# Kernel optimization log

Measured on AMD Instinct MI355X. Metric: run time of the kernel, lower is better.

The kernel has to match this reference:

```python
import jax, jax.numpy as jnp
import numpy as np

N_POINTS = 8388608  # 8M points


def setup_inputs() -> dict:
    key = jax.random.key(0)
    k1, k2 = jax.random.split(key)
    pcloud = jax.random.normal(k1, (1, N_POINTS, 3), dtype=jnp.float32)
    P1 = jax.random.normal(k2, (3,), dtype=jnp.float32)
    return {"pcloud": pcloud, "P1": P1, "K": 64}


def reference(pcloud, P1, K):
    # pcloud: (1, N, 3) -> (N, 3); P1: (3,) -> (1, 3)
    pts = pcloud.reshape(-1, 3)
    diff = pts - P1.reshape(1, 3)
    dist = jnp.sqrt(jnp.sum(diff * diff, axis=1))  # L2 distance per point, (N,)
    # torch.topk(largest=False) == top_k on negated distances
    _, idx = jax.lax.top_k(-dist, K)  # (K,)
    return pts[idx], idx.reshape(1, -1)
```

## Files before the change

kernel.cpp:

```cpp
#include <hip/hip_runtime.h>
#include <stdint.h>

#define NBINS 4096
#define NB2   4096
#define NBLK  2048
#define SLOT  16
#define OVF_CAP 8192
#define LDS_CAND 8192
#define SAMP_PTS 131072
#define CHUNK_PTS 256
#define CHUNK_F4  192

__device__ __forceinline__ uint32_t dist_key(float x, float y, float z,
                                             float px, float py, float pz) {
    float dx = __fsub_rn(x, px);
    float dy = __fsub_rn(y, py);
    float dz = __fsub_rn(z, pz);
    float s = __fadd_rn(__fadd_rn(__fmul_rn(dx, dx), __fmul_rn(dy, dy)),
                        __fmul_rn(dz, dz));
    float d = __fsqrt_rn(s);
    return __float_as_uint(d);
}

__global__ void __launch_bounds__(256) sample_hist_kernel(const float* __restrict__ pts,
                                                          const float* __restrict__ P1,
                                                          uint32_t* __restrict__ ghist,
                                                          int nsamp) {
    __shared__ uint32_t lh[NBINS];
    for (int i = threadIdx.x; i < NBINS; i += 256) lh[i] = 0;
    __syncthreads();
    float px = P1[0], py = P1[1], pz = P1[2];
    int gid = blockIdx.x * 256 + threadIdx.x;
    const float4* p4 = (const float4*)pts;
    if (gid * 4 < nsamp) {
        float4 A = p4[gid * 3 + 0];
        float4 Bv = p4[gid * 3 + 1];
        float4 Cv = p4[gid * 3 + 2];
        atomicAdd(&lh[dist_key(A.x, A.y, A.z, px, py, pz) >> 20], 1u);
        atomicAdd(&lh[dist_key(A.w, Bv.x, Bv.y, px, py, pz) >> 20], 1u);
        atomicAdd(&lh[dist_key(Bv.z, Bv.w, Cv.x, px, py, pz) >> 20], 1u);
        atomicAdd(&lh[dist_key(Cv.y, Cv.z, Cv.w, px, py, pz) >> 20], 1u);
    }
    __syncthreads();
    for (int i = threadIdx.x; i < NBINS; i += 256) {
        uint32_t v = lh[i];
        if (v) atomicAdd(&ghist[i], v);
    }
}

__global__ void __launch_bounds__(256) scan_kernel(const uint32_t* __restrict__ ghist,
                                                   uint32_t* __restrict__ cut, int K) {
    __shared__ uint32_t s[256];
    int t = threadIdx.x;
    uint32_t mine[16];
    uint32_t local = 0;
    for (int j = 0; j < 16; ++j) {
        mine[j] = ghist[t * 16 + j];
        local += mine[j];
    }
    s[t] = local;
    __syncthreads();
    for (int off = 1; off < 256; off <<= 1) {
        uint32_t v = (t >= off) ? s[t - off] : 0;
        __syncthreads();
        s[t] += v;
        __syncthreads();
    }
    uint32_t incl = s[t];
    uint32_t excl = incl - local;
    if (excl < (uint32_t)K && incl >= (uint32_t)K) {
        uint32_t run = excl;
        for (int j = 0; j < 16; ++j) {
            run += mine[j];
            if (run >= (uint32_t)K) {
                *cut = (uint32_t)(t * 16 + j);
                break;
            }
        }
    }
}

__global__ void __launch_bounds__(256) filter6_kernel(const float* __restrict__ pts,
                                                      const float* __restrict__ P1,
                                                      const uint32_t* __restrict__ cut,
                                                      unsigned long long* __restrict__ gslots,
                                                      uint32_t* __restrict__ gcount,
                                                      uint32_t* __restrict__ ovf_cnt,
                                                      unsigned long long* __restrict__ ovf,
                                                      int nchunks, int N) {
    __shared__ float4 park[4][CHUNK_F4];
    __shared__ unsigned long long lhits[SLOT];
    __shared__ uint32_t lcnt;
    if (threadIdx.x == 0) lcnt = 0;
    __syncthreads();

    const float4* p4 = (const float4*)pts;
    float px = P1[0], py = P1[1], pz = P1[2];
    uint32_t cb = *cut;
    int w = threadIdx.x >> 6;
    int lane = threadIdx.x & 63;
    int b = blockIdx.x;
    int cpb = (nchunks + NBLK - 1) / NBLK;
    int cbeg = b * cpb;
    int cend = cbeg + cpb; if (cend > nchunks) cend = nchunks;

    float4 r0, r1, r2;
    int c = cbeg + w;
    if (c < cend) {
        const float4* s = p4 + (size_t)c * CHUNK_F4;
        r0 = s[lane]; r1 = s[lane + 64]; r2 = s[lane + 128];
    }
    for (; c < cend; c += 4) {
        park[w][lane] = r0;
        park[w][lane + 64] = r1;
        park[w][lane + 128] = r2;
        int cn = c + 4;
        if (cn < cend) {
            const float4* s = p4 + (size_t)cn * CHUNK_F4;
            r0 = s[lane]; r1 = s[lane + 64]; r2 = s[lane + 128];
        }
        asm volatile("s_waitcnt lgkmcnt(0)" ::: "memory");
        const float* fb = (const float*)&park[w][0] + lane * 12;
        float4 A  = *(const float4*)(fb);
        float4 Bv = *(const float4*)(fb + 4);
        float4 Cv = *(const float4*)(fb + 8);
        uint32_t kk[4];
        kk[0] = dist_key(A.x, A.y, A.z, px, py, pz);
        kk[1] = dist_key(A.w, Bv.x, Bv.y, px, py, pz);
        kk[2] = dist_key(Bv.z, Bv.w, Cv.x, px, py, pz);
        kk[3] = dist_key(Cv.y, Cv.z, Cv.w, px, py, pz);
        uint32_t pbase = (uint32_t)c * CHUNK_PTS + (uint32_t)lane * 4;
        #pragma unroll
        for (int j = 0; j < 4; ++j) {
            if ((kk[j] >> 20) <= cb) {
                unsigned long long cv = ((unsigned long long)kk[j] << 32) |
                                        (unsigned long long)(pbase + j);
                uint32_t pos = atomicAdd(&lcnt, 1u);
                if (pos < SLOT) {
                    lhits[pos] = cv;
                } else {
                    uint32_t op = atomicAdd(ovf_cnt, 1u);
                    if (op < OVF_CAP) ovf[op] = cv;
                }
            }
        }
    }
    if (b == NBLK - 1 && threadIdx.x == 0) {
        for (int i = nchunks * CHUNK_PTS; i < N; ++i) {
            uint32_t kk = dist_key(pts[3 * i], pts[3 * i + 1], pts[3 * i + 2], px, py, pz);
            if ((kk >> 20) <= cb) {
                unsigned long long cv = ((unsigned long long)kk << 32) |
                                        (unsigned long long)(uint32_t)i;
                uint32_t pos = atomicAdd(&lcnt, 1u);
                if (pos < SLOT) {
                    lhits[pos] = cv;
                } else {
                    uint32_t op = atomicAdd(ovf_cnt, 1u);
                    if (op < OVF_CAP) ovf[op] = cv;
                }
            }
        }
    }
    __syncthreads();
    uint32_t n = lcnt; if (n > SLOT) n = SLOT;
    if (threadIdx.x < n) gslots[(size_t)b * SLOT + threadIdx.x] = lhits[threadIdx.x];
    if (threadIdx.x == 0) gcount[b] = n;
}

__global__ void __launch_bounds__(1024) refine_select_kernel(
        const uint32_t* __restrict__ gcount,
        const unsigned long long* __restrict__ gslots,
        const uint32_t* __restrict__ ovf_cnt,
        const unsigned long long* __restrict__ ovf,
        const uint32_t* __restrict__ cut,
        unsigned long long* __restrict__ cand2,
        const float* __restrict__ pts,
        float* __restrict__ out, int K) {
    __shared__ uint32_t hist2[NB2];
    __shared__ uint32_t ssum[1024];
    __shared__ unsigned long long lcand[LDS_CAND];
    __shared__ uint32_t cut2_s, m2_s;
    int t = threadIdx.x;
    uint32_t cb = *cut;
    unsigned long long R = ((unsigned long long)(cb + 1)) << 20;
    uint32_t M32 = (uint32_t)((((unsigned long long)NB2) << 32) / R);
    uint32_t novf = *ovf_cnt; if (novf > OVF_CAP) novf = OVF_CAP;

    for (int i = t; i < NB2; i += 1024) hist2[i] = 0;
    if (t == 0) m2_s = 0;
    __syncthreads();
    for (int b = t; b < NBLK; b += 1024) {
        uint32_t n = gcount[b];
        for (uint32_t j = 0; j < n; ++j) {
            uint32_t key = (uint32_t)(gslots[(size_t)b * SLOT + j] >> 32);
            atomicAdd(&hist2[(uint32_t)(((unsigned long long)key * M32) >> 32)], 1u);
        }
    }
    for (uint32_t i = t; i < novf; i += 1024) {
        uint32_t key = (uint32_t)(ovf[i] >> 32);
        atomicAdd(&hist2[(uint32_t)(((unsigned long long)key * M32) >> 32)], 1u);
    }
    __syncthreads();

    uint32_t mine[4];
    uint32_t local = 0;
    for (int j = 0; j < 4; ++j) { mine[j] = hist2[t * 4 + j]; local += mine[j]; }
    ssum[t] = local;
    __syncthreads();
    for (int off = 1; off < 1024; off <<= 1) {
        uint32_t v = (t >= off) ? ssum[t - off] : 0;
        __syncthreads();
        ssum[t] += v;
        __syncthreads();
    }
    uint32_t incl = ssum[t], excl = incl - local;
    if (excl < (uint32_t)K && incl >= (uint32_t)K) {
        uint32_t run = excl;
        for (int j = 0; j < 4; ++j) {
            run += mine[j];
            if (run >= (uint32_t)K) { cut2_s = (uint32_t)(t * 4 + j); break; }
        }
    }
    __syncthreads();
    uint32_t c2 = cut2_s;

    for (int b = t; b < NBLK; b += 1024) {
        uint32_t n = gcount[b];
        for (uint32_t j = 0; j < n; ++j) {
            unsigned long long cv = gslots[(size_t)b * SLOT + j];
            uint32_t key = (uint32_t)(cv >> 32);
            if ((uint32_t)(((unsigned long long)key * M32) >> 32) <= c2) {
                uint32_t pos = atomicAdd(&m2_s, 1u);
                if (pos < LDS_CAND) lcand[pos] = cv;
                cand2[pos] = cv;
            }
        }
    }
    for (uint32_t i = t; i < novf; i += 1024) {
        unsigned long long cv = ovf[i];
        uint32_t key = (uint32_t)(cv >> 32);
        if ((uint32_t)(((unsigned long long)key * M32) >> 32) <= c2) {
            uint32_t pos = atomicAdd(&m2_s, 1u);
            if (pos < LDS_CAND) lcand[pos] = cv;
            cand2[pos] = cv;
        }
    }
    __syncthreads();
    uint32_t M2 = m2_s;

    if (M2 <= LDS_CAND) {
        for (uint32_t i = t; i < M2; i += 1024) {
            unsigned long long ci = lcand[i];
            uint32_t rank = 0;
            for (uint32_t j = 0; j < M2; ++j) rank += (lcand[j] < ci) ? 1u : 0u;
            if (rank < (uint32_t)K) {
                uint32_t idx = (uint32_t)(ci & 0xFFFFFFFFu);
                out[3 * rank + 0] = pts[3 * idx + 0];
                out[3 * rank + 1] = pts[3 * idx + 1];
                out[3 * rank + 2] = pts[3 * idx + 2];
                out[3 * K + rank] = (float)idx;
            }
        }
    } else {
        for (uint32_t i = t; i < M2; i += 1024) {
            unsigned long long ci = cand2[i];
            uint32_t rank = 0;
            for (uint32_t j = 0; j < M2; ++j) rank += (cand2[j] < ci) ? 1u : 0u;
            if (rank < (uint32_t)K) {
                uint32_t idx = (uint32_t)(ci & 0xFFFFFFFFu);
                out[3 * rank + 0] = pts[3 * idx + 0];
                out[3 * rank + 1] = pts[3 * idx + 1];
                out[3 * rank + 2] = pts[3 * idx + 2];
                out[3 * K + rank] = (float)idx;
            }
        }
    }
}

extern "C" void kernel_launch(void* const* d_in, const int* in_sizes, int n_in,
                              void* d_out, int out_size, void* d_ws, size_t ws_size,
                              hipStream_t stream) {
    const float* pts = (const float*)d_in[0];
    const float* P1  = (const float*)d_in[1];
    float* out = (float*)d_out;

    int N = in_sizes[0] / 3;
    int nchunks = N / CHUNK_PTS;
    int K = out_size / 4;
    int nsamp = (N < SAMP_PTS) ? (N / 4) * 4 : SAMP_PTS;

    uint32_t* w       = (uint32_t*)d_ws;
    uint32_t* ovf_cnt = w + 0;
    uint32_t* cut     = w + 1;
    uint32_t* hist    = w + 4;
    uint32_t* gcount  = w + 4 + NBINS;
    unsigned long long* gslots = (unsigned long long*)(w + 4 + NBINS + NBLK);
    unsigned long long* ovf    = gslots + (size_t)NBLK * SLOT;
    unsigned long long* cand2  = ovf + OVF_CAP;

    hipMemsetAsync(w, 0, (size_t)(4 + NBINS + NBLK) * sizeof(uint32_t), stream);
    sample_hist_kernel<<<(nsamp / 4 + 255) / 256, 256, 0, stream>>>(pts, P1, hist, nsamp);
    scan_kernel<<<1, 256, 0, stream>>>(hist, cut, K);
    filter6_kernel<<<NBLK, 256, 0, stream>>>(pts, P1, cut, gslots, gcount, ovf_cnt, ovf, nchunks, N);
    refine_select_kernel<<<1, 1024, 0, stream>>>(gcount, gslots, ovf_cnt, ovf, cut,
                                                 cand2, pts, out, K);
}
```

Baseline: 45.16 us.

## Fuse scan into sampling and refine into filter via last-block atomic counters

Merges the single-block scan into the sampling kernel and the single-block refine/select into the filter kernel. The last block to finish, found through an atomic done counter, runs the follow-up work, which cuts the launch count from four to two and removes the gaps between dependent kernels. The refine stage now runs with 256 threads instead of 1024, uses a smaller second histogram and a smaller LDS candidate buffer, and reuses the parking LDS through a shared byte array. This risks a slower tail phase and a more frequent fallback to the global candidate array.

```diff
diff --git a/kernel.cpp b/kernel.cpp
--- a/kernel.cpp
+++ b/kernel.cpp
@@ -2,12 +2,14 @@
 #include <stdint.h>
 
 #define NBINS 4096
-#define NB2   4096
+#define NB2   2048
 #define NBLK  2048
 #define SLOT  16
 #define OVF_CAP 8192
-#define LDS_CAND 8192
+#define CAND2_CAP 8192
+#define LDS_CAND2 1024
 #define SAMP_PTS 131072
+#define SBLK 128
 #define CHUNK_PTS 256
 #define CHUNK_F4  192
 
@@ -22,11 +24,13 @@
     return __float_as_uint(d);
 }
 
-__global__ void __launch_bounds__(256) sample_hist_kernel(const float* __restrict__ pts,
-                                                          const float* __restrict__ P1,
-                                                          uint32_t* __restrict__ ghist,
-                                                          int nsamp) {
+__global__ void __launch_bounds__(256) sample_scan_kernel(
+        const float* __restrict__ pts, const float* __restrict__ P1,
+        uint32_t* __restrict__ ghist, uint32_t* __restrict__ cutp,
+        uint32_t* __restrict__ done_s, int nsamp, int K) {
     __shared__ uint32_t lh[NBINS];
+    __shared__ uint32_t ssum[256];
+    __shared__ int is_last;
     for (int i = threadIdx.x; i < NBINS; i += 256) lh[i] = 0;
     __syncthreads();
     float px = P1[0], py = P1[1], pz = P1[2];
@@ -46,57 +50,67 @@
         uint32_t v = lh[i];
         if (v) atomicAdd(&ghist[i], v);
     }
-}
-
-__global__ void __launch_bounds__(256) scan_kernel(const uint32_t* __restrict__ ghist,
-                                                   uint32_t* __restrict__ cut, int K) {
-    __shared__ uint32_t s[256];
+    __syncthreads();
+    if (threadIdx.x == 0) {
+        __threadfence();
+        uint32_t old = __hip_atomic_fetch_add(done_s, 1u, __ATOMIC_ACQ_REL,
+                                              __HIP_MEMORY_SCOPE_AGENT);
+        is_last = (old == (uint32_t)(gridDim.x - 1));
+    }
+    __syncthreads();
+    if (!is_last) return;
+    __threadfence();
+
     int t = threadIdx.x;
     uint32_t mine[16];
     uint32_t local = 0;
     for (int j = 0; j < 16; ++j) {
-        mine[j] = ghist[t * 16 + j];
+        mine[j] = __hip_atomic_load(&ghist[t * 16 + j], __ATOMIC_RELAXED,
+                                    __HIP_MEMORY_SCOPE_AGENT);
         local += mine[j];
     }
-    s[t] = local;
+    ssum[t] = local;
     __syncthreads();
     for (int off = 1; off < 256; off <<= 1) {
-        uint32_t v = (t >= off) ? s[t - off] : 0;
+        uint32_t v = (t >= off) ? ssum[t - off] : 0;
         __syncthreads();
-        s[t] += v;
+        ssum[t] += v;
         __syncthreads();
     }
-    uint32_t incl = s[t];
+    uint32_t incl = ssum[t];
     uint32_t excl = incl - local;
     if (excl < (uint32_t)K && incl >= (uint32_t)K) {
         uint32_t run = excl;
         for (int j = 0; j < 16; ++j) {
             run += mine[j];
-            if (run >= (uint32_t)K) {
-                *cut = (uint32_t)(t * 16 + j);
-                break;
-            }
+            if (run >= (uint32_t)K) { *cutp = (uint32_t)(t * 16 + j); break; }
         }
     }
 }
 
-__global__ void __launch_bounds__(256) filter6_kernel(const float* __restrict__ pts,
-                                                      const float* __restrict__ P1,
-                                                      const uint32_t* __restrict__ cut,
-                                                      unsigned long long* __restrict__ gslots,
-                                                      uint32_t* __restrict__ gcount,
-                                                      uint32_t* __restrict__ ovf_cnt,
-                                                      unsigned long long* __restrict__ ovf,
-                                                      int nchunks, int N) {
-    __shared__ float4 park[4][CHUNK_F4];
+__global__ void __launch_bounds__(256) filter_refine_kernel(
+        const float* __restrict__ pts, const float* __restrict__ P1,
+        const uint32_t* __restrict__ cutp,
+        unsigned long long* __restrict__ gslots,
+        uint32_t* __restrict__ gcount,
+        uint32_t* __restrict__ ovf_cnt, unsigned long long* __restrict__ ovf,
+        uint32_t* __restrict__ done_f,
+        unsigned long long* __restrict__ cand2,
+        float* __restrict__ out,
+        int nchunks, int N, int K) {
+    __shared__ __align__(16) unsigned char smem[17472];
     __shared__ unsigned long long lhits[SLOT];
     __shared__ uint32_t lcnt;
+    __shared__ int is_last;
+    __shared__ uint32_t cut2_s, m2_s;
+    float4 (*park)[CHUNK_F4] = (float4 (*)[CHUNK_F4])smem;
+
     if (threadIdx.x == 0) lcnt = 0;
     __syncthreads();
 
     const float4* p4 = (const float4*)pts;
     float px = P1[0], py = P1[1], pz = P1[2];
-    uint32_t cb = *cut;
+    uint32_t cb = *cutp;
     int w = threadIdx.x >> 6;
     int lane = threadIdx.x & 63;
     int b = blockIdx.x;
@@ -164,50 +178,54 @@
     __syncthreads();
     uint32_t n = lcnt; if (n > SLOT) n = SLOT;
     if (threadIdx.x < n) gslots[(size_t)b * SLOT + threadIdx.x] = lhits[threadIdx.x];
-    if (threadIdx.x == 0) gcount[b] = n;
-}
-
-__global__ void __launch_bounds__(1024) refine_select_kernel(
-        const uint32_t* __restrict__ gcount,
-        const unsigned long long* __restrict__ gslots,
-        const uint32_t* __restrict__ ovf_cnt,
-        const unsigned long long* __restrict__ ovf,
-        const uint32_t* __restrict__ cut,
-        unsigned long long* __restrict__ cand2,
-        const float* __restrict__ pts,
-        float* __restrict__ out, int K) {
-    __shared__ uint32_t hist2[NB2];
-    __shared__ uint32_t ssum[1024];
-    __shared__ unsigned long long lcand[LDS_CAND];
-    __shared__ uint32_t cut2_s, m2_s;
+    if (threadIdx.x == 0)
+        __hip_atomic_store(&gcount[b], n, __ATOMIC_RELAXED, __HIP_MEMORY_SCOPE_AGENT);
+
+    __syncthreads();
+    if (threadIdx.x == 0) {
+        __threadfence();
+        uint32_t old = __hip_atomic_fetch_add(done_f, 1u, __ATOMIC_ACQ_REL,
+                                              __HIP_MEMORY_SCOPE_AGENT);
+        is_last = (old == (uint32_t)(NBLK - 1));
+    }
+    __syncthreads();
+    if (!is_last) return;
+    __threadfence();
+
+    uint32_t* hist2 = (uint32_t*)smem;
+    uint32_t* ssum  = (uint32_t*)(smem + 8192);
+    unsigned long long* lc = (unsigned long long*)(smem + 9216);
     int t = threadIdx.x;
-    uint32_t cb = *cut;
     unsigned long long R = ((unsigned long long)(cb + 1)) << 20;
     uint32_t M32 = (uint32_t)((((unsigned long long)NB2) << 32) / R);
-    uint32_t novf = *ovf_cnt; if (novf > OVF_CAP) novf = OVF_CAP;
-
-    for (int i = t; i < NB2; i += 1024) hist2[i] = 0;
-    if (t == 0) m2_s = 0;
-    __syncthreads();
-    for (int b = t; b < NBLK; b += 1024) {
-        uint32_t n = gcount[b];
-        for (uint32_t j = 0; j < n; ++j) {
-            uint32_t key = (uint32_t)(gslots[(size_t)b * SLOT + j] >> 32);
+    uint32_t novf = __hip_atomic_load(ovf_cnt, __ATOMIC_RELAXED,
+                                      __HIP_MEMORY_SCOPE_AGENT);
+    if (novf > OVF_CAP) novf = OVF_CAP;
+
+    for (int i = t; i < NB2; i += 256) hist2[i] = 0;
+    if (t == 0) { m2_s = 0; cut2_s = NB2 - 1; }
+    __syncthreads();
+    for (int bb = t; bb < NBLK; bb += 256) {
+        uint32_t nn = __hip_atomic_load(&gcount[bb], __ATOMIC_RELAXED,
+                                        __HIP_MEMORY_SCOPE_AGENT);
+        if (nn > SLOT) nn = SLOT;
+        for (uint32_t j = 0; j < nn; ++j) {
+            uint32_t key = (uint32_t)(gslots[(size_t)bb * SLOT + j] >> 32);
             atomicAdd(&hist2[(uint32_t)(((unsigned long long)key * M32) >> 32)], 1u);
         }
     }
-    for (uint32_t i = t; i < novf; i += 1024) {
+    for (uint32_t i = t; i < novf; i += 256) {
         uint32_t key = (uint32_t)(ovf[i] >> 32);
         atomicAdd(&hist2[(uint32_t)(((unsigned long long)key * M32) >> 32)], 1u);
     }
     __syncthreads();
 
-    uint32_t mine[4];
+    uint32_t mine[8];
     uint32_t local = 0;
-    for (int j = 0; j < 4; ++j) { mine[j] = hist2[t * 4 + j]; local += mine[j]; }
+    for (int j = 0; j < 8; ++j) { mine[j] = hist2[t * 8 + j]; local += mine[j]; }
     ssum[t] = local;
     __syncthreads();
-    for (int off = 1; off < 1024; off <<= 1) {
+    for (int off = 1; off < 256; off <<= 1) {
         uint32_t v = (t >= off) ? ssum[t - off] : 0;
         __syncthreads();
         ssum[t] += v;
@@ -216,43 +234,45 @@
     uint32_t incl = ssum[t], excl = incl - local;
     if (excl < (uint32_t)K && incl >= (uint32_t)K) {
         uint32_t run = excl;
-        for (int j = 0; j < 4; ++j) {
+        for (int j = 0; j < 8; ++j) {
             run += mine[j];
-            if (run >= (uint32_t)K) { cut2_s = (uint32_t)(t * 4 + j); break; }
+            if (run >= (uint32_t)K) { cut2_s = (uint32_t)(t * 8 + j); break; }
         }
     }
     __syncthreads();
     uint32_t c2 = cut2_s;
 
-    for (int b = t; b < NBLK; b += 1024) {
-        uint32_t n = gcount[b];
-        for (uint32_t j = 0; j < n; ++j) {
-            unsigned long long cv = gslots[(size_t)b * SLOT + j];
+    for (int bb = t; bb < NBLK; bb += 256) {
+        uint32_t nn = __hip_atomic_load(&gcount[bb], __ATOMIC_RELAXED,
+                                        __HIP_MEMORY_SCOPE_AGENT);
+        if (nn > SLOT) nn = SLOT;
+        for (uint32_t j = 0; j < nn; ++j) {
+            unsigned long long cv = gslots[(size_t)bb * SLOT + j];
             uint32_t key = (uint32_t)(cv >> 32);
             if ((uint32_t)(((unsigned long long)key * M32) >> 32) <= c2) {
                 uint32_t pos = atomicAdd(&m2_s, 1u);
-                if (pos < LDS_CAND) lcand[pos] = cv;
-                cand2[pos] = cv;
-            }
-        }
-    }
-    for (uint32_t i = t; i < novf; i += 1024) {
+                if (pos < LDS_CAND2) lc[pos] = cv;
+                if (pos < CAND2_CAP) cand2[pos] = cv;
+            }
+        }
+    }
+    for (uint32_t i = t; i < novf; i += 256) {
         unsigned long long cv = ovf[i];
         uint32_t key = (uint32_t)(cv >> 32);
         if ((uint32_t)(((unsigned long long)key * M32) >> 32) <= c2) {
             uint32_t pos = atomicAdd(&m2_s, 1u);
-            if (pos < LDS_CAND) lcand[pos] = cv;
-            cand2[pos] = cv;
+            if (pos < LDS_CAND2) lc[pos] = cv;
+            if (pos < CAND2_CAP) cand2[pos] = cv;
         }
     }
     __syncthreads();
     uint32_t M2 = m2_s;
 
-    if (M2 <= LDS_CAND) {
-        for (uint32_t i = t; i < M2; i += 1024) {
-            unsigned long long ci = lcand[i];
+    if (M2 <= LDS_CAND2) {
+        for (uint32_t i = t; i < M2; i += 256) {
+            unsigned long long ci = lc[i];
             uint32_t rank = 0;
-            for (uint32_t j = 0; j < M2; ++j) rank += (lcand[j] < ci) ? 1u : 0u;
+            for (uint32_t j = 0; j < M2; ++j) rank += (lc[j] < ci) ? 1u : 0u;
             if (rank < (uint32_t)K) {
                 uint32_t idx = (uint32_t)(ci & 0xFFFFFFFFu);
                 out[3 * rank + 0] = pts[3 * idx + 0];
@@ -262,7 +282,8 @@
             }
         }
     } else {
-        for (uint32_t i = t; i < M2; i += 1024) {
+        if (M2 > CAND2_CAP) M2 = CAND2_CAP;
+        for (uint32_t i = t; i < M2; i += 256) {
             unsigned long long ci = cand2[i];
             uint32_t rank = 0;
             for (uint32_t j = 0; j < M2; ++j) rank += (cand2[j] < ci) ? 1u : 0u;
@@ -290,18 +311,19 @@
     int nsamp = (N < SAMP_PTS) ? (N / 4) * 4 : SAMP_PTS;
 
     uint32_t* w       = (uint32_t*)d_ws;
-    uint32_t* ovf_cnt = w + 0;
-    uint32_t* cut     = w + 1;
-    uint32_t* hist    = w + 4;
-    uint32_t* gcount  = w + 4 + NBINS;
-    unsigned long long* gslots = (unsigned long long*)(w + 4 + NBINS + NBLK);
+    uint32_t* hist    = w;
+    uint32_t* ovf_cnt = w + NBINS;
+    uint32_t* done_s  = w + NBINS + 1;
+    uint32_t* done_f  = w + NBINS + 2;
+    uint32_t* cutp    = w + NBINS + 3;
+    uint32_t* gcount  = w + NBINS + 8;
+    unsigned long long* gslots = (unsigned long long*)(w + NBINS + 8 + NBLK);
     unsigned long long* ovf    = gslots + (size_t)NBLK * SLOT;
     unsigned long long* cand2  = ovf + OVF_CAP;
 
-    hipMemsetAsync(w, 0, (size_t)(4 + NBINS + NBLK) * sizeof(uint32_t), stream);
-    sample_hist_kernel<<<(nsamp / 4 + 255) / 256, 256, 0, stream>>>(pts, P1, hist, nsamp);
-    scan_kernel<<<1, 256, 0, stream>>>(hist, cut, K);
-    filter6_kernel<<<NBLK, 256, 0, stream>>>(pts, P1, cut, gslots, gcount, ovf_cnt, ovf, nchunks, N);
-    refine_select_kernel<<<1, 1024, 0, stream>>>(gcount, gslots, ovf_cnt, ovf, cut,
-                                                 cand2, pts, out, K);
+    hipMemsetAsync(w, 0, (size_t)(NBINS + 4) * sizeof(uint32_t), stream);
+    sample_scan_kernel<<<SBLK, 256, 0, stream>>>(pts, P1, hist, cutp, done_s, nsamp, K);
+    filter_refine_kernel<<<NBLK, 256, 0, stream>>>(pts, P1, cutp, gslots, gcount,
+                                                   ovf_cnt, ovf, done_f, cand2,
+                                                   out, nchunks, N, K);
 }
```

Result: slower. 163.4 us (+261.8%).

## Fuse sample histogram with scan via last-block pattern and double-buffer filter loads

Applied to the files above, without the earlier changes.

The separate scan kernel is folded into the sampling kernel: the last block to finish, detected with an atomic done counter, performs the prefix scan and writes the cut bin. This removes one kernel launch and its dependency gap. The filter loop now keeps two chunks of register prefetch in flight (A and B buffers) instead of one, to hide more global-memory latency at the cost of extra registers. It also shrinks the memset, clamps gcount reads, and initialises cut2_s defensively.

```diff
diff --git a/kernel.cpp b/kernel.cpp
--- a/kernel.cpp
+++ b/kernel.cpp
@@ -8,6 +8,7 @@
 #define OVF_CAP 8192
 #define LDS_CAND 8192
 #define SAMP_PTS 131072
+#define SBLK 128
 #define CHUNK_PTS 256
 #define CHUNK_F4  192
 
@@ -22,11 +23,13 @@
     return __float_as_uint(d);
 }
 
-__global__ void __launch_bounds__(256) sample_hist_kernel(const float* __restrict__ pts,
-                                                          const float* __restrict__ P1,
-                                                          uint32_t* __restrict__ ghist,
-                                                          int nsamp) {
+__global__ void __launch_bounds__(256) sample_scan_kernel(
+        const float* __restrict__ pts, const float* __restrict__ P1,
+        uint32_t* __restrict__ ghist, uint32_t* __restrict__ cutp,
+        uint32_t* __restrict__ done_s, int nsamp, int K) {
     __shared__ uint32_t lh[NBINS];
+    __shared__ uint32_t ssum[256];
+    __shared__ int is_last;
     for (int i = threadIdx.x; i < NBINS; i += 256) lh[i] = 0;
     __syncthreads();
     float px = P1[0], py = P1[1], pz = P1[2];
@@ -46,48 +49,50 @@
         uint32_t v = lh[i];
         if (v) atomicAdd(&ghist[i], v);
     }
-}
-
-__global__ void __launch_bounds__(256) scan_kernel(const uint32_t* __restrict__ ghist,
-                                                   uint32_t* __restrict__ cut, int K) {
-    __shared__ uint32_t s[256];
+    __syncthreads();
+    if (threadIdx.x == 0) {
+        asm volatile("s_waitcnt vmcnt(0)" ::: "memory");
+        uint32_t old = __hip_atomic_fetch_add(done_s, 1u, __ATOMIC_RELAXED,
+                                              __HIP_MEMORY_SCOPE_AGENT);
+        is_last = (old == (uint32_t)(gridDim.x - 1));
+    }
+    __syncthreads();
+    if (!is_last) return;
+
     int t = threadIdx.x;
     uint32_t mine[16];
     uint32_t local = 0;
     for (int j = 0; j < 16; ++j) {
-        mine[j] = ghist[t * 16 + j];
+        mine[j] = __hip_atomic_load(&ghist[t * 16 + j], __ATOMIC_RELAXED,
+                                    __HIP_MEMORY_SCOPE_AGENT);
         local += mine[j];
     }
-    s[t] = local;
+    ssum[t] = local;
     __syncthreads();
     for (int off = 1; off < 256; off <<= 1) {
-        uint32_t v = (t >= off) ? s[t - off] : 0;
+        uint32_t v = (t >= off) ? ssum[t - off] : 0;
         __syncthreads();
-        s[t] += v;
+        ssum[t] += v;
         __syncthreads();
     }
-    uint32_t incl = s[t];
+    uint32_t incl = ssum[t];
     uint32_t excl = incl - local;
     if (excl < (uint32_t)K && incl >= (uint32_t)K) {
         uint32_t run = excl;
         for (int j = 0; j < 16; ++j) {
             run += mine[j];
-            if (run >= (uint32_t)K) {
-                *cut = (uint32_t)(t * 16 + j);
-                break;
-            }
-        }
-    }
-}
-
-__global__ void __launch_bounds__(256) filter6_kernel(const float* __restrict__ pts,
-                                                      const float* __restrict__ P1,
-                                                      const uint32_t* __restrict__ cut,
-                                                      unsigned long long* __restrict__ gslots,
-                                                      uint32_t* __restrict__ gcount,
-                                                      uint32_t* __restrict__ ovf_cnt,
-                                                      unsigned long long* __restrict__ ovf,
-                                                      int nchunks, int N) {
+            if (run >= (uint32_t)K) { *cutp = (uint32_t)(t * 16 + j); break; }
+        }
+    }
+}
+
+__global__ void __launch_bounds__(256) filter_kernel(
+        const float* __restrict__ pts, const float* __restrict__ P1,
+        const uint32_t* __restrict__ cutp,
+        unsigned long long* __restrict__ gslots,
+        uint32_t* __restrict__ gcount,
+        uint32_t* __restrict__ ovf_cnt, unsigned long long* __restrict__ ovf,
+        int nchunks, int N) {
     __shared__ float4 park[4][CHUNK_F4];
     __shared__ unsigned long long lhits[SLOT];
     __shared__ uint32_t lcnt;
@@ -96,7 +101,7 @@
 
     const float4* p4 = (const float4*)pts;
     float px = P1[0], py = P1[1], pz = P1[2];
-    uint32_t cb = *cut;
+    uint32_t cb = *cutp;
     int w = threadIdx.x >> 6;
     int lane = threadIdx.x & 63;
     int b = blockIdx.x;
@@ -104,46 +109,87 @@
     int cbeg = b * cpb;
     int cend = cbeg + cpb; if (cend > nchunks) cend = nchunks;
 
-    float4 r0, r1, r2;
+    float4 a0, a1, a2, b0, b1, b2;
     int c = cbeg + w;
-    if (c < cend) {
+    bool hasA = (c < cend);
+    if (hasA) {
         const float4* s = p4 + (size_t)c * CHUNK_F4;
-        r0 = s[lane]; r1 = s[lane + 64]; r2 = s[lane + 128];
-    }
-    for (; c < cend; c += 4) {
-        park[w][lane] = r0;
-        park[w][lane + 64] = r1;
-        park[w][lane + 128] = r2;
-        int cn = c + 4;
-        if (cn < cend) {
-            const float4* s = p4 + (size_t)cn * CHUNK_F4;
-            r0 = s[lane]; r1 = s[lane + 64]; r2 = s[lane + 128];
+        a0 = s[lane]; a1 = s[lane + 64]; a2 = s[lane + 128];
+    }
+    bool hasB = (c + 4 < cend);
+    if (hasB) {
+        const float4* s = p4 + (size_t)(c + 4) * CHUNK_F4;
+        b0 = s[lane]; b1 = s[lane + 64]; b2 = s[lane + 128];
+    }
+    while (hasA) {
+        park[w][lane] = a0; park[w][lane + 64] = a1; park[w][lane + 128] = a2;
+        bool loadA = (c + 8 < cend);
+        if (loadA) {
+            const float4* s = p4 + (size_t)(c + 8) * CHUNK_F4;
+            a0 = s[lane]; a1 = s[lane + 64]; a2 = s[lane + 128];
         }
         asm volatile("s_waitcnt lgkmcnt(0)" ::: "memory");
-        const float* fb = (const float*)&park[w][0] + lane * 12;
-        float4 A  = *(const float4*)(fb);
-        float4 Bv = *(const float4*)(fb + 4);
-        float4 Cv = *(const float4*)(fb + 8);
-        uint32_t kk[4];
-        kk[0] = dist_key(A.x, A.y, A.z, px, py, pz);
-        kk[1] = dist_key(A.w, Bv.x, Bv.y, px, py, pz);
-        kk[2] = dist_key(Bv.z, Bv.w, Cv.x, px, py, pz);
-        kk[3] = dist_key(Cv.y, Cv.z, Cv.w, px, py, pz);
-        uint32_t pbase = (uint32_t)c * CHUNK_PTS + (uint32_t)lane * 4;
-        #pragma unroll
-        for (int j = 0; j < 4; ++j) {
-            if ((kk[j] >> 20) <= cb) {
-                unsigned long long cv = ((unsigned long long)kk[j] << 32) |
-                                        (unsigned long long)(pbase + j);
-                uint32_t pos = atomicAdd(&lcnt, 1u);
-                if (pos < SLOT) {
-                    lhits[pos] = cv;
-                } else {
-                    uint32_t op = atomicAdd(ovf_cnt, 1u);
-                    if (op < OVF_CAP) ovf[op] = cv;
+        {
+            const float* fb = (const float*)&park[w][0] + lane * 12;
+            float4 A  = *(const float4*)(fb);
+            float4 Bv = *(const float4*)(fb + 4);
+            float4 Cv = *(const float4*)(fb + 8);
+            uint32_t kk[4];
+            kk[0] = dist_key(A.x, A.y, A.z, px, py, pz);
+            kk[1] = dist_key(A.w, Bv.x, Bv.y, px, py, pz);
+            kk[2] = dist_key(Bv.z, Bv.w, Cv.x, px, py, pz);
+            kk[3] = dist_key(Cv.y, Cv.z, Cv.w, px, py, pz);
+            uint32_t pbase = (uint32_t)c * CHUNK_PTS + (uint32_t)lane * 4;
+            #pragma unroll
+            for (int j = 0; j < 4; ++j) {
+                if ((kk[j] >> 20) <= cb) {
+                    unsigned long long cv = ((unsigned long long)kk[j] << 32) |
+                                            (unsigned long long)(pbase + j);
+                    uint32_t pos = atomicAdd(&lcnt, 1u);
+                    if (pos < SLOT) lhits[pos] = cv;
+                    else {
+                        uint32_t op = atomicAdd(ovf_cnt, 1u);
+                        if (op < OVF_CAP) ovf[op] = cv;
+                    }
                 }
             }
         }
+        bool loadB = false;
+        if (hasB) {
+            park[w][lane] = b0; park[w][lane + 64] = b1; park[w][lane + 128] = b2;
+            loadB = (c + 12 < cend);
+            if (loadB) {
+                const float4* s = p4 + (size_t)(c + 12) * CHUNK_F4;
+                b0 = s[lane]; b1 = s[lane + 64]; b2 = s[lane + 128];
+            }
+            asm volatile("s_waitcnt lgkmcnt(0)" ::: "memory");
+            const float* fb = (const float*)&park[w][0] + lane * 12;
+            float4 A  = *(const float4*)(fb);
+            float4 Bv = *(const float4*)(fb + 4);
+            float4 Cv = *(const float4*)(fb + 8);
+            uint32_t kk[4];
+            kk[0] = dist_key(A.x, A.y, A.z, px, py, pz);
+            kk[1] = dist_key(A.w, Bv.x, Bv.y, px, py, pz);
+            kk[2] = dist_key(Bv.z, Bv.w, Cv.x, px, py, pz);
+            kk[3] = dist_key(Cv.y, Cv.z, Cv.w, px, py, pz);
+            uint32_t pbase = (uint32_t)(c + 4) * CHUNK_PTS + (uint32_t)lane * 4;
+            #pragma unroll
+            for (int j = 0; j < 4; ++j) {
+                if ((kk[j] >> 20) <= cb) {
+                    unsigned long long cv = ((unsigned long long)kk[j] << 32) |
+                                            (unsigned long long)(pbase + j);
+                    uint32_t pos = atomicAdd(&lcnt, 1u);
+                    if (pos < SLOT) lhits[pos] = cv;
+                    else {
+                        uint32_t op = atomicAdd(ovf_cnt, 1u);
+                        if (op < OVF_CAP) ovf[op] = cv;
+                    }
+                }
+            }
+        }
+        c += 8;
+        hasA = (c < cend);
+        hasB = loadB;
     }
     if (b == NBLK - 1 && threadIdx.x == 0) {
         for (int i = nchunks * CHUNK_PTS; i < N; ++i) {
@@ -152,9 +198,8 @@
                 unsigned long long cv = ((unsigned long long)kk << 32) |
                                         (unsigned long long)(uint32_t)i;
                 uint32_t pos = atomicAdd(&lcnt, 1u);
-                if (pos < SLOT) {
-                    lhits[pos] = cv;
-                } else {
+                if (pos < SLOT) lhits[pos] = cv;
+                else {
                     uint32_t op = atomicAdd(ovf_cnt, 1u);
                     if (op < OVF_CAP) ovf[op] = cv;
                 }
@@ -172,7 +217,7 @@
         const unsigned long long* __restrict__ gslots,
         const uint32_t* __restrict__ ovf_cnt,
         const unsigned long long* __restrict__ ovf,
-        const uint32_t* __restrict__ cut,
+        const uint32_t* __restrict__ cutp,
         unsigned long long* __restrict__ cand2,
         const float* __restrict__ pts,
         float* __restrict__ out, int K) {
@@ -181,16 +226,16 @@
     __shared__ unsigned long long lcand[LDS_CAND];
     __shared__ uint32_t cut2_s, m2_s;
     int t = threadIdx.x;
-    uint32_t cb = *cut;
+    uint32_t cb = *cutp;
     unsigned long long R = ((unsigned long long)(cb + 1)) << 20;
     uint32_t M32 = (uint32_t)((((unsigned long long)NB2) << 32) / R);
     uint32_t novf = *ovf_cnt; if (novf > OVF_CAP) novf = OVF_CAP;
 
     for (int i = t; i < NB2; i += 1024) hist2[i] = 0;
-    if (t == 0) m2_s = 0;
+    if (t == 0) { m2_s = 0; cut2_s = NB2 - 1; }
     __syncthreads();
     for (int b = t; b < NBLK; b += 1024) {
-        uint32_t n = gcount[b];
+        uint32_t n = gcount[b]; if (n > SLOT) n = SLOT;
         for (uint32_t j = 0; j < n; ++j) {
             uint32_t key = (uint32_t)(gslots[(size_t)b * SLOT + j] >> 32);
             atomicAdd(&hist2[(uint32_t)(((unsigned long long)key * M32) >> 32)], 1u);
@@ -225,7 +270,7 @@
     uint32_t c2 = cut2_s;
 
     for (int b = t; b < NBLK; b += 1024) {
-        uint32_t n = gcount[b];
+        uint32_t n = gcount[b]; if (n > SLOT) n = SLOT;
         for (uint32_t j = 0; j < n; ++j) {
             unsigned long long cv = gslots[(size_t)b * SLOT + j];
             uint32_t key = (uint32_t)(cv >> 32);
@@ -291,17 +336,18 @@
 
     uint32_t* w       = (uint32_t*)d_ws;
     uint32_t* ovf_cnt = w + 0;
-    uint32_t* cut     = w + 1;
+    uint32_t* cutp    = w + 1;
+    uint32_t* done_s  = w + 2;
     uint32_t* hist    = w + 4;
     uint32_t* gcount  = w + 4 + NBINS;
     unsigned long long* gslots = (unsigned long long*)(w + 4 + NBINS + NBLK);
     unsigned long long* ovf    = gslots + (size_t)NBLK * SLOT;
     unsigned long long* cand2  = ovf + OVF_CAP;
 
-    hipMemsetAsync(w, 0, (size_t)(4 + NBINS + NBLK) * sizeof(uint32_t), stream);
-    sample_hist_kernel<<<(nsamp / 4 + 255) / 256, 256, 0, stream>>>(pts, P1, hist, nsamp);
-    scan_kernel<<<1, 256, 0, stream>>>(hist, cut, K);
-    filter6_kernel<<<NBLK, 256, 0, stream>>>(pts, P1, cut, gslots, gcount, ovf_cnt, ovf, nchunks, N);
-    refine_select_kernel<<<1, 1024, 0, stream>>>(gcount, gslots, ovf_cnt, ovf, cut,
-                                                 cand2, pts, out, K);
-}
+    hipMemsetAsync(w, 0, (size_t)(4 + NBINS) * sizeof(uint32_t), stream);
+    sample_scan_kernel<<<SBLK, 256, 0, stream>>>(pts, P1, hist, cutp, done_s, nsamp, K);
+    filter_kernel<<<NBLK, 256, 0, stream>>>(pts, P1, cutp, gslots, gcount,
+                                            ovf_cnt, ovf, nchunks, N);
+    refine_select_kernel<<<1, 1024, 0, stream>>>(gcount, gslots, ovf_cnt, ovf,
+                                                 cutp, cand2, pts, out, K);
+}
```

Result: slower. 47.94 us (+6.2%).
